# Kernel tuning notes

Measured on AMD Instinct MI355X. Metric: run time of the kernel, lower is better.

Reference implementation:

```python
import jax, jax.numpy as jnp
import numpy as np

VOXEL_SIZE = 96
SHARPNESS = 100.0
EPS = 1e-8


def _grid_coords(V):
    # matches torch: x fastest, normalized by (V-1); shape [V*V, 2] as (x, y)
    y, x = jnp.meshgrid(jnp.arange(V, dtype=jnp.float32), jnp.arange(V, dtype=jnp.float32), indexing='ij')
    return jnp.stack([x.ravel(), y.ravel()], axis=1) / float(V - 1)


def setup_inputs() -> dict:
    key = jax.random.key(0)
    k1, k2, k3 = jax.random.split(key, 3)
    B, N, P = 4, 32, 32
    polygons = jax.random.uniform(k1, (B, N, P, 2), dtype=jnp.float32)
    attributes = jax.random.uniform(k2, (B, 8), dtype=jnp.float32)
    validity_scores = jax.random.uniform(k3, (B, N), dtype=jnp.float32)
    return {"polygons": polygons, "attributes": attributes, "validity_scores": validity_scores}


def _polygon_masks(polygons, coords):
    # polygons: [B,N,P,2], coords: [M,2] -> soft occupancy masks [B,N,M]
    v0 = polygons                              # [B,N,P,2]
    v1 = jnp.roll(polygons, -1, axis=2)        # next vertex (closed loop)
    e = v1 - v0                                # edges [B,N,P,2]
    pts = coords[None, None, None]             # [1,1,1,M,2]
    v = pts - v0[:, :, :, None, :]             # [B,N,P,M,2]
    e_sq = (e * e).sum(-1) + EPS               # [B,N,P]
    t = (v * e[:, :, :, None, :]).sum(-1) / e_sq[..., None]   # [B,N,P,M]
    t = jnp.clip(t, 0.0, 1.0)
    proj = v0[:, :, :, None, :] + t[..., None] * e[:, :, :, None, :]
    diff = pts - proj
    dists = jnp.sqrt((diff * diff).sum(-1))    # [B,N,P,M]
    min_dist = dists.min(axis=2)               # [B,N,M] min over edges
    # ray-casting point-in-polygon (horizontal ray toward +x)
    x_pts = coords[:, 0]                        # [M]
    y_pts = coords[:, 1]
    x0, y0 = v0[..., 0:1], v0[..., 1:2]        # [B,N,P,1]
    x1, y1 = v1[..., 0:1], v1[..., 1:2]
    y_crosses = ((y0 <= y_pts) & (y1 > y_pts)) | ((y1 <= y_pts) & (y0 > y_pts))
    inter_x = x0 + (x1 - x0) * ((y_pts - y0) / (y1 - y0 + EPS))
    crossings = (inter_x > x_pts) & y_crosses  # [B,N,P,M]
    inside = (crossings.sum(axis=2) % 2) == 1  # [B,N,M]
    sdf = jnp.where(inside, -min_dist, min_dist)
    return jax.nn.sigmoid(-sdf * SHARPNESS)    # [B,N,M]


def reference(polygons, attributes, validity_scores):
    B = polygons.shape[0]
    V = VOXEL_SIZE
    coords = _grid_coords(V)                                   # [V*V, 2]
    masks = _polygon_masks(polygons, coords)                   # [B,N,M]
    valid = validity_scores >= 0.5                             # [B,N]
    combined = jnp.max(jnp.where(valid[:, :, None], masks, 0.0), axis=1)  # [B,M]
    combined = combined.reshape(B, V, V)                       # [B,H,W]
    # height extrusion: int(round(clamp(attr,0,1)*D)), clamped to [1,D]; non-differentiable
    norm_h = jnp.clip(attributes[:, 0], 0.0, 1.0)
    hv = jnp.clip(jnp.round(norm_h * V), 1.0, float(V))        # [B]
    hv = jax.lax.stop_gradient(hv)
    depth_mask = (jnp.arange(V, dtype=jnp.float32)[None, :] < hv[:, None]).astype(combined.dtype)  # [B,D]
    voxels = combined[:, None, :, :] * depth_mask[:, :, None, None]  # [B,D,H,W]
    return voxels
```

## Files before the change

kernel.cpp:

```cpp
#include <hip/hip_runtime.h>

#define V 96
#define VV (V * V)
#define B_ 4
#define N_ 32
#define P_ 32
#define TILES (VV / 256)

__global__ __launch_bounds__(256) void mask_kernel(
    const float* __restrict__ poly,
    const float* __restrict__ validity,
    float* __restrict__ partial)
{
    const int bn  = blockIdx.x / TILES;
    const int pix = (blockIdx.x % TILES) * 256 + threadIdx.x;

    if (validity[bn] < 0.5f) return;

    __shared__ float4 sE[P_][2];
    if (threadIdx.x < P_) {
        const int p  = threadIdx.x;
        const int pn = (p + 1) & (P_ - 1);
        const float* base = poly + (size_t)bn * (P_ * 2);
        float x0 = base[p * 2],  y0 = base[p * 2 + 1];
        float x1 = base[pn * 2], y1 = base[pn * 2 + 1];
        float ex = x1 - x0, ey = y1 - y0;
        float srq = __builtin_amdgcn_rcpf(ex * ex + ey * ey + 1e-8f);
        float sry = __builtin_amdgcn_rcpf(ey + 1e-8f);
        float sI  = ex * sry;
        float cI  = fmaf(-sI, y0, x0);
        sE[p][0] = make_float4(x0, y0, ex, ey);
        sE[p][1] = make_float4(srq, y1, cI, sI);
    }
    __syncthreads();

    const int py_i = pix / V, px_i = pix - py_i * V;
    const float px = (float)px_i / 95.0f;
    const float py = (float)py_i / 95.0f;

    float mind2 = 1e30f;
    int   par   = 0;
    #pragma unroll
    for (int p = 0; p < P_; ++p) {
        const float4 e0 = sE[p][0];
        const float4 e1 = sE[p][1];

        float vx = px - e0.x, vy = py - e0.y;
        float t  = (vx * e0.z + vy * e0.w) * e1.x;
        t = fminf(fmaxf(t, 0.0f), 1.0f);
        float dx = fmaf(-t, e0.z, vx), dy = fmaf(-t, e0.w, vy);
        float d2 = fmaf(dx, dx, dy * dy);
        mind2 = fminf(mind2, d2);

        bool c0 = (e0.y <= py);
        bool c1 = (e1.y <= py);
        float ix = fmaf(e1.w, py, e1.z);
        par ^= (int)((c0 != c1) & (ix > px));
    }
    float mind = sqrtf(mind2);
    float sdf  = par ? -mind : mind;
    float m = __builtin_amdgcn_rcpf(1.0f + __builtin_amdgcn_exp2f(sdf * 144.26950408889634f));

    partial[(size_t)bn * VV + pix] = m;
}

__global__ __launch_bounds__(192) void expand_kernel(
    const float* __restrict__ partial,
    const float* __restrict__ validity,
    const float* __restrict__ attr,
    float4* __restrict__ out)
{
    const int bid = blockIdx.x;
    const int b   = bid / (V * 4);
    const int rem = bid - b * (V * 4);
    const int y   = rem >> 2;
    const int q   = rem & 3;
    const int t   = threadIdx.x;

    __shared__ float red[V];

    if (t < V) {
        const int x = t;
        float m = 0.0f;
        #pragma unroll
        for (int n = 0; n < N_; ++n) {
            if (validity[b * N_ + n] >= 0.5f) {
                m = fmaxf(m, partial[(size_t)(b * N_ + n) * VV + y * V + x]);
            }
        }
        red[x] = m;
    }
    __syncthreads();

    float a  = attr[b * 8];
    float nh = fminf(fmaxf(a, 0.0f), 1.0f);
    float hv = fminf(fmaxf(rintf(nh * (float)V), 1.0f), (float)V);

    const float4* red4 = (const float4*)red;
    #pragma unroll
    for (int it = 0; it < 3; ++it) {
        const int idx = it * 192 + t;
        const int dl  = idx / 24;
        const int x4  = idx - dl * 24;
        const int d   = q * 24 + dl;
        const float keep = ((float)d < hv) ? 1.0f : 0.0f;
        float4 c = red4[x4];
        out[((size_t)(b * V + d) * V + y) * (V / 4) + x4] =
            make_float4(c.x * keep, c.y * keep, c.z * keep, c.w * keep);
    }
}

extern "C" void kernel_launch(void* const* d_in, const int* in_sizes, int n_in,
                              void* d_out, int out_size, void* d_ws, size_t ws_size,
                              hipStream_t stream) {
    const float* polygons = (const float*)d_in[0];
    const float* attrs    = (const float*)d_in[1];
    const float* validity = (const float*)d_in[2];
    float* out     = (float*)d_out;
    float* partial = (float*)d_ws;

    mask_kernel<<<B_ * N_ * TILES, 256, 0, stream>>>(polygons, validity, partial);
    expand_kernel<<<B_ * V * 4, 192, 0, stream>>>(partial, validity, attrs, (float4*)out);
}
```

Before: 79.16 us.

## Fuse mask computation, polygon max-reduction and depth extrusion into one kernel

The mask and expand kernels are merged into a single kernel. Each block covers 64 pixels of one batch and stages all 32 polygons' edge data in shared memory. Each wave evaluates 4 polygons, the per-pixel max is reduced with a shared atomicMax on the float bits, and the block then writes all 96 depth slices directly. This drops the intermediate partial buffer and the second launch. In exchange the grid is smaller (576 blocks), output stores are scalar rather than float4, and each block stages 32KB of shared memory.

```diff
diff --git a/kernel.cpp b/kernel.cpp
--- a/kernel.cpp
+++ b/kernel.cpp
@@ -5,23 +5,33 @@
 #define B_ 4
 #define N_ 32
 #define P_ 32
-#define TILES (VV / 256)
+#define TPB 512
+#define PXB 64
+#define TILES_PER_B (VV / PXB)
+#define WAVES (TPB / 64)
+#define NPW (N_ / WAVES)
+#define DPW (V / WAVES)
 
-__global__ __launch_bounds__(256) void mask_kernel(
+__global__ __launch_bounds__(TPB) void fused_kernel(
     const float* __restrict__ poly,
+    const float* __restrict__ attr,
     const float* __restrict__ validity,
-    float* __restrict__ partial)
+    float* __restrict__ out)
 {
-    const int bn  = blockIdx.x / TILES;
-    const int pix = (blockIdx.x % TILES) * 256 + threadIdx.x;
+    const int b    = blockIdx.x / TILES_PER_B;
+    const int tile = blockIdx.x % TILES_PER_B;
+    const int t    = threadIdx.x;
+    const int wave = t >> 6;
+    const int lane = t & 63;
 
-    if (validity[bn] < 0.5f) return;
+    __shared__ float4 sE[N_][P_][2];
+    __shared__ unsigned int red[PXB];
 
-    __shared__ float4 sE[P_][2];
-    if (threadIdx.x < P_) {
-        const int p  = threadIdx.x;
-        const int pn = (p + 1) & (P_ - 1);
-        const float* base = poly + (size_t)bn * (P_ * 2);
+    if (t < PXB) red[t] = 0u;
+
+    for (int k = t; k < N_ * P_; k += TPB) {
+        const int n = k >> 5, p = k & 31, pn = (p + 1) & 31;
+        const float* base = poly + (size_t)(b * N_ + n) * (P_ * 2);
         float x0 = base[p * 2],  y0 = base[p * 2 + 1];
         float x1 = base[pn * 2], y1 = base[pn * 2 + 1];
         float ex = x1 - x0, ey = y1 - y0;
@@ -29,84 +39,59 @@
         float sry = __builtin_amdgcn_rcpf(ey + 1e-8f);
         float sI  = ex * sry;
         float cI  = fmaf(-sI, y0, x0);
-        sE[p][0] = make_float4(x0, y0, ex, ey);
-        sE[p][1] = make_float4(srq, y1, cI, sI);
+        sE[n][p][0] = make_float4(x0, y0, ex, ey);
+        sE[n][p][1] = make_float4(srq, y1, cI, sI);
     }
     __syncthreads();
 
+    const int pix  = tile * PXB + lane;
     const int py_i = pix / V, px_i = pix - py_i * V;
     const float px = (float)px_i / 95.0f;
     const float py = (float)py_i / 95.0f;
 
-    float mind2 = 1e30f;
-    int   par   = 0;
+    float best = 0.0f;
     #pragma unroll
-    for (int p = 0; p < P_; ++p) {
-        const float4 e0 = sE[p][0];
-        const float4 e1 = sE[p][1];
+    for (int i = 0; i < NPW; ++i) {
+        const int n = wave * NPW + i;
+        if (validity[b * N_ + n] < 0.5f) continue;
 
-        float vx = px - e0.x, vy = py - e0.y;
-        float t  = (vx * e0.z + vy * e0.w) * e1.x;
-        t = fminf(fmaxf(t, 0.0f), 1.0f);
-        float dx = fmaf(-t, e0.z, vx), dy = fmaf(-t, e0.w, vy);
-        float d2 = fmaf(dx, dx, dy * dy);
-        mind2 = fminf(mind2, d2);
+        float mind2 = 1e30f;
+        int   par   = 0;
+        #pragma unroll
+        for (int p = 0; p < P_; ++p) {
+            const float4 e0 = sE[n][p][0];
+            const float4 e1 = sE[n][p][1];
 
-        bool c0 = (e0.y <= py);
-        bool c1 = (e1.y <= py);
-        float ix = fmaf(e1.w, py, e1.z);
-        par ^= (int)((c0 != c1) & (ix > px));
+            float vx = px - e0.x, vy = py - e0.y;
+            float tt = (vx * e0.z + vy * e0.w) * e1.x;
+            tt = fminf(fmaxf(tt, 0.0f), 1.0f);
+            float dx = fmaf(-tt, e0.z, vx), dy = fmaf(-tt, e0.w, vy);
+            mind2 = fminf(mind2, fmaf(dx, dx, dy * dy));
+
+            bool c0 = (e0.y <= py);
+            bool c1 = (e1.y <= py);
+            float ix = fmaf(e1.w, py, e1.z);
+            par ^= (int)((c0 != c1) & (ix > px));
+        }
+        float mind = sqrtf(mind2);
+        float sdf  = par ? -mind : mind;
+        float m = __builtin_amdgcn_rcpf(
+            1.0f + __builtin_amdgcn_exp2f(sdf * 144.26950408889634f));
+        best = fmaxf(best, m);
     }
-    float mind = sqrtf(mind2);
-    float sdf  = par ? -mind : mind;
-    float m = __builtin_amdgcn_rcpf(1.0f + __builtin_amdgcn_exp2f(sdf * 144.26950408889634f));
-
-    partial[(size_t)bn * VV + pix] = m;
-}
-
-__global__ __launch_bounds__(192) void expand_kernel(
-    const float* __restrict__ partial,
-    const float* __restrict__ validity,
-    const float* __restrict__ attr,
-    float4* __restrict__ out)
-{
-    const int bid = blockIdx.x;
-    const int b   = bid / (V * 4);
-    const int rem = bid - b * (V * 4);
-    const int y   = rem >> 2;
-    const int q   = rem & 3;
-    const int t   = threadIdx.x;
-
-    __shared__ float red[V];
-
-    if (t < V) {
-        const int x = t;
-        float m = 0.0f;
-        #pragma unroll
-        for (int n = 0; n < N_; ++n) {
-            if (validity[b * N_ + n] >= 0.5f) {
-                m = fmaxf(m, partial[(size_t)(b * N_ + n) * VV + y * V + x]);
-            }
-        }
-        red[x] = m;
-    }
+    atomicMax(&red[lane], __float_as_uint(best));
     __syncthreads();
 
-    float a  = attr[b * 8];
-    float nh = fminf(fmaxf(a, 0.0f), 1.0f);
-    float hv = fminf(fmaxf(rintf(nh * (float)V), 1.0f), (float)V);
-
-    const float4* red4 = (const float4*)red;
+    const float a  = attr[b * 8];
+    const float nh = fminf(fmaxf(a, 0.0f), 1.0f);
+    const float hv = fminf(fmaxf(rintf(nh * (float)V), 1.0f), (float)V);
+    const float c  = __uint_as_float(red[lane]);
+    float* obase = out + (size_t)b * V * VV + tile * PXB + lane;
     #pragma unroll
-    for (int it = 0; it < 3; ++it) {
-        const int idx = it * 192 + t;
-        const int dl  = idx / 24;
-        const int x4  = idx - dl * 24;
-        const int d   = q * 24 + dl;
+    for (int i = 0; i < DPW; ++i) {
+        const int d = wave * DPW + i;
         const float keep = ((float)d < hv) ? 1.0f : 0.0f;
-        float4 c = red4[x4];
-        out[((size_t)(b * V + d) * V + y) * (V / 4) + x4] =
-            make_float4(c.x * keep, c.y * keep, c.z * keep, c.w * keep);
+        obase[(size_t)d * VV] = c * keep;
     }
 }
 
@@ -116,9 +101,7 @@
     const float* polygons = (const float*)d_in[0];
     const float* attrs    = (const float*)d_in[1];
     const float* validity = (const float*)d_in[2];
-    float* out     = (float*)d_out;
-    float* partial = (float*)d_ws;
+    float* out = (float*)d_out;
 
-    mask_kernel<<<B_ * N_ * TILES, 256, 0, stream>>>(polygons, validity, partial);
-    expand_kernel<<<B_ * V * 4, 192, 0, stream>>>(partial, validity, attrs, (float4*)out);
+    fused_kernel<<<B_ * TILES_PER_B, TPB, 0, stream>>>(polygons, attrs, validity, out);
 }
```

After: 74.54 us. 5.8% less time.
